# Kernel tuning notes

Hardware: AMD Instinct MI355X
Metric: run time of the kernel (lower is better)

Reference implementation:

```python
import jax, jax.numpy as jnp
import numpy as np
from jax import lax

B, T, IN, H, NCLASS = 256, 512, 64, 128, 6
SCALE = 0.05


def setup_inputs() -> dict:
    key = jax.random.key(0)
    ks = jax.random.split(key, 9)
    return {
        "x": jax.random.normal(ks[0], (B, T, IN), jnp.float32),
        "w_ih0": jax.random.normal(ks[1], (3 * H, IN), jnp.float32) * SCALE,
        "w_ih1": jax.random.normal(ks[2], (3 * H, H), jnp.float32) * SCALE,
        "w_ih2": jax.random.normal(ks[3], (3 * H, H), jnp.float32) * SCALE,
        "w_hh": jax.random.normal(ks[4], (3, 3 * H, H), jnp.float32) * SCALE,
        "b_ih": jax.random.normal(ks[5], (3, 3 * H), jnp.float32) * SCALE,
        "b_hh": jax.random.normal(ks[6], (3, 3 * H), jnp.float32) * SCALE,
        "fc_w": jax.random.normal(ks[7], (NCLASS, H), jnp.float32) * SCALE,
        "fc_b": jax.random.normal(ks[8], (NCLASS,), jnp.float32) * SCALE,
    }


def _gru_layer(x, w_ih, w_hh, b_ih, b_hh):
    # x: [B, T, in]; PyTorch gate order: r, z, n
    gx = jnp.einsum("bti,gi->btg", x, w_ih) + b_ih          # [B, T, 3H]
    gx_r, gx_z, gx_n = jnp.split(gx, 3, axis=-1)
    w_hr, w_hz, w_hn = jnp.split(w_hh, 3, axis=0)           # each [H, H]
    b_hr, b_hz, b_hn = jnp.split(b_hh, 3)

    def step(h, g):
        gr, gz, gn = g
        r = jax.nn.sigmoid(gr + h @ w_hr.T + b_hr)
        z = jax.nn.sigmoid(gz + h @ w_hz.T + b_hz)
        n = jnp.tanh(gn + r * (h @ w_hn.T + b_hn))
        h_new = (1.0 - z) * n + z * h
        return h_new, h_new

    h0 = jnp.zeros((x.shape[0], w_hh.shape[1]), x.dtype)
    xs = (gx_r.transpose(1, 0, 2), gx_z.transpose(1, 0, 2), gx_n.transpose(1, 0, 2))
    _, hs = lax.scan(step, h0, xs)                          # hs: [T, B, H]
    return hs.transpose(1, 0, 2)                            # [B, T, H]


def reference(x, w_ih0, w_ih1, w_ih2, w_hh, b_ih, b_hh, fc_w, fc_b):
    h = _gru_layer(x, w_ih0, w_hh[0], b_ih[0], b_hh[0])
    h = _gru_layer(h, w_ih1, w_hh[1], b_ih[1], b_hh[1])
    h = _gru_layer(h, w_ih2, w_hh[2], b_ih[2], b_hh[2])
    last = h[:, -1, :]                                      # [B, H]
    # Dropout2d(0.25) is identity in eval mode.
    return last @ fc_w.T + fc_b                             # [B, NCLASS]
```

## Files before the change

kernel.cpp:

```cpp
#include <hip/hip_runtime.h>
#include <stdint.h>


#define B_   256
#define T_   512
#define IN_  64
#define H_   128
#define G_   384

typedef short bf16x8 __attribute__((ext_vector_type(8)));
typedef float f32x4  __attribute__((ext_vector_type(4)));
typedef unsigned long long u64x2 __attribute__((ext_vector_type(2)));

__device__ __forceinline__ unsigned short f2bf(float f) {
  union { float f; unsigned u; } v; v.f = f;
  unsigned u = v.u;
  u += 0x7fffu + ((u >> 16) & 1u);
  return (unsigned short)(u >> 16);
}
__device__ __forceinline__ float bf2f(unsigned short h) {
  union { unsigned u; float f; } v; v.u = ((unsigned)h) << 16; return v.f;
}

__device__ __forceinline__ void gload16(const void* g, void* l) {
  __builtin_amdgcn_global_load_lds(
      (const __attribute__((address_space(1))) void*)g,
      (__attribute__((address_space(3))) void*)l, 16, 0, 0);
}

template <int K, bool AF32>
__global__ __launch_bounds__(512) void gemm_gx(const void* __restrict__ Ap,
                                               const float* __restrict__ W,
                                               unsigned short* __restrict__ gx) {
  __shared__ __align__(16) unsigned short smem[(128 + G_) * K];
  unsigned short* lA = smem;
  unsigned short* lW = smem + 128 * K;
  const int tid = threadIdx.x;
  const int m0 = blockIdx.x * 128;

  if (AF32) {
    const float* A = (const float*)Ap;
    const int nch = 128 * K / 4;
    for (int c = tid; c < nch; c += 512) {
      int row = c / (K / 4), kq = c - row * (K / 4);
      float4 v = *(const float4*)(A + (size_t)(m0 + row) * K + kq * 4);
      unsigned long long pk = (unsigned long long)f2bf(v.x) |
                              ((unsigned long long)f2bf(v.y) << 16) |
                              ((unsigned long long)f2bf(v.z) << 32) |
                              ((unsigned long long)f2bf(v.w) << 48);
      unsigned byte = ((unsigned)(row * K + kq * 4) * 2u) ^ (((unsigned)row & 7u) << 4);
      *(unsigned long long*)((char*)lA + byte) = pk;
    }
  } else {
    const unsigned short* A = (const unsigned short*)Ap;
    const int nch = 128 * K / 8;
    for (int c = tid; c < nch; c += 512) {
      int row = c / (K / 8), ko = c - row * (K / 8);
      bf16x8 v = *(const bf16x8*)(A + (size_t)(m0 + row) * K + ko * 8);
      unsigned byte = ((unsigned)(row * K + ko * 8) * 2u) ^ (((unsigned)row & 7u) << 4);
      *(bf16x8*)((char*)lA + byte) = v;
    }
  }
  {
    const int nch = G_ * K / 4;
    for (int c = tid; c < nch; c += 512) {
      int g = c / (K / 4), kq = c - g * (K / 4);
      float4 v = *(const float4*)(W + (size_t)g * K + kq * 4);
      unsigned long long pk = (unsigned long long)f2bf(v.x) |
                              ((unsigned long long)f2bf(v.y) << 16) |
                              ((unsigned long long)f2bf(v.z) << 32) |
                              ((unsigned long long)f2bf(v.w) << 48);
      unsigned byte = ((unsigned)(g * K + kq * 4) * 2u) ^ (((unsigned)g & 7u) << 4);
      *(unsigned long long*)((char*)lW + byte) = pk;
    }
  }
  __syncthreads();

  const int l = tid & 63, w = tid >> 6;
  const int rg = w >> 2, cg = w & 3;
  const int lr = l & 15, g4 = l >> 4;

  f32x4 acc[4][6];
#pragma unroll
  for (int i = 0; i < 4; ++i)
#pragma unroll
    for (int j = 0; j < 6; ++j) acc[i][j] = (f32x4){0.f, 0.f, 0.f, 0.f};

#pragma unroll
  for (int ks = 0; ks < K / 32; ++ks) {
    bf16x8 a[4];
#pragma unroll
    for (int i = 0; i < 4; ++i) {
      int row = (rg * 4 + i) * 16 + lr;
      unsigned byte = ((unsigned)(row * K + ks * 32 + g4 * 8) * 2u) ^ (((unsigned)row & 7u) << 4);
      a[i] = *(const bf16x8*)((const char*)lA + byte);
    }
#pragma unroll
    for (int j = 0; j < 6; ++j) {
      int g = (cg * 6 + j) * 16 + lr;
      unsigned byte = ((unsigned)(g * K + ks * 32 + g4 * 8) * 2u) ^ (((unsigned)g & 7u) << 4);
      bf16x8 bfr = *(const bf16x8*)((const char*)lW + byte);
#pragma unroll
      for (int i = 0; i < 4; ++i)
        acc[i][j] = __builtin_amdgcn_mfma_f32_16x16x32_bf16(a[i], bfr, acc[i][j], 0, 0, 0);
    }
  }

  unsigned short* lC = smem;
#pragma unroll
  for (int half = 0; half < 2; ++half) {
    __syncthreads();
    if (rg == half) {
#pragma unroll
      for (int i = 0; i < 4; ++i)
#pragma unroll
        for (int j = 0; j < 6; ++j)
#pragma unroll
          for (int r = 0; r < 4; ++r) {
            int mloc = i * 16 + g4 * 4 + r;
            int g = (cg * 6 + j) * 16 + lr;
            lC[mloc * 388 + g] = f2bf(acc[i][j][r]);
          }
    }
    __syncthreads();
    for (int it = 0; it < 6; ++it) {
      int c = tid + it * 512;
      int mloc = c / 48, cb = c - mloc * 48;
      unsigned long long lo =
          *(const unsigned long long*)((const char*)lC + mloc * 776 + cb * 16);
      unsigned long long hi =
          *(const unsigned long long*)((const char*)lC + mloc * 776 + cb * 16 + 8);
      int m = m0 + half * 64 + mloc;
      int row;
      if (AF32) { int t = m & 511, b = m >> 9; row = t * 256 + b; }
      else      { row = m; }
      u64x2 v; v[0] = lo; v[1] = hi;
      *(u64x2*)((char*)gx + (size_t)row * (G_ * 2) + cb * 16) = v;
    }
  }
}

template <int DOSEQ, int DOFC>
__global__ __launch_bounds__(512) void gru_scan(
    const unsigned short* __restrict__ gx,
    const float* __restrict__ Whh,
    const float* __restrict__ bih,
    const float* __restrict__ bhh,
    unsigned short* __restrict__ hseq,
    const float* __restrict__ fcw,
    const float* __restrict__ fcb,
    float* __restrict__ out) {
  __shared__ __align__(16) unsigned short lh[2][2048];
  __shared__ __align__(16) unsigned short lgx[4][1536];

  const int tid = threadIdx.x, l = tid & 63, w = tid >> 6;
  const int lr = l & 15, g4 = l >> 4;
  const int b0 = blockIdx.x * 4;
  const int batch = g4;
  const int hcol = w * 16 + lr;

  for (int i = tid; i < 4096; i += 512) ((unsigned short*)lh)[i] = 0;

  const float c_r  = bih[hcol]           + bhh[hcol];
  const float c_z  = bih[128 + hcol]     + bhh[128 + hcol];
  const float c_n1 = bih[256 + hcol];
  const float c_n2 = bhh[256 + hcol];

  bf16x8 Bf[3][4];
#pragma unroll
  for (int ci = 0; ci < 3; ++ci) {
    int gcol = (w + ci * 8) * 16 + lr;
#pragma unroll
    for (int ks = 0; ks < 4; ++ks) {
      const float* p = Whh + (size_t)gcol * H_ + ks * 32 + g4 * 8;
      float4 v0 = *(const float4*)p;
      float4 v1 = *(const float4*)(p + 4);
      bf16x8 f;
      f[0] = (short)f2bf(v0.x); f[1] = (short)f2bf(v0.y);
      f[2] = (short)f2bf(v0.z); f[3] = (short)f2bf(v0.w);
      f[4] = (short)f2bf(v1.x); f[5] = (short)f2bf(v1.y);
      f[6] = (short)f2bf(v1.z); f[7] = (short)f2bf(v1.w);
      Bf[ci][ks] = f;
    }
  }

  __syncthreads();
  if (w < 3) {
#pragma unroll
    for (int p = 0; p < 3; ++p) {
      const char* src = (const char*)gx + ((size_t)(p * 256 + b0) * G_) * 2 + (size_t)tid * 16;
      gload16(src, (char*)&lgx[p][0] + w * 1024);
    }
    asm volatile("s_waitcnt vmcnt(2)" ::: "memory");
  }
  asm volatile("s_waitcnt lgkmcnt(0)" ::: "memory");
  __builtin_amdgcn_s_barrier();
  __builtin_amdgcn_sched_barrier(0);

  float hreg = 0.f;

  for (int t = 0; t < T_; ++t) {
    const int cur = t & 1, nxt = cur ^ 1;
    const int slot = t & 3;

    bf16x8 a[4];
#pragma unroll
    for (int ks = 0; ks < 4; ++ks) {
      unsigned byte = ((unsigned)(lr * 256 + ks * 64 + g4 * 16)) ^ (((unsigned)lr & 7u) << 4);
      a[ks] = *(const bf16x8*)((const char*)lh[cur] + byte);
    }
    const float gxr = bf2f(lgx[slot][batch * G_ + hcol]);
    const float gxz = bf2f(lgx[slot][batch * G_ + 128 + hcol]);
    const float gxn = bf2f(lgx[slot][batch * G_ + 256 + hcol]);

    f32x4 aR = (f32x4){0.f, 0.f, 0.f, 0.f};
    f32x4 aZ = (f32x4){0.f, 0.f, 0.f, 0.f};
    f32x4 aN = (f32x4){0.f, 0.f, 0.f, 0.f};
#pragma unroll
    for (int ks = 0; ks < 4; ++ks) {
      aR = __builtin_amdgcn_mfma_f32_16x16x32_bf16(a[ks], Bf[0][ks], aR, 0, 0, 0);
      aZ = __builtin_amdgcn_mfma_f32_16x16x32_bf16(a[ks], Bf[1][ks], aZ, 0, 0, 0);
      aN = __builtin_amdgcn_mfma_f32_16x16x32_bf16(a[ks], Bf[2][ks], aN, 0, 0, 0);
    }

    float hWr, hWz, hWn;
    {
      float y0 = __shfl(aR[0], lr, 64), y1 = __shfl(aR[1], lr, 64);
      float y2 = __shfl(aR[2], lr, 64), y3 = __shfl(aR[3], lr, 64);
      hWr = batch == 0 ? y0 : batch == 1 ? y1 : batch == 2 ? y2 : y3;
    }
    {
      float y0 = __shfl(aZ[0], lr, 64), y1 = __shfl(aZ[1], lr, 64);
      float y2 = __shfl(aZ[2], lr, 64), y3 = __shfl(aZ[3], lr, 64);
      hWz = batch == 0 ? y0 : batch == 1 ? y1 : batch == 2 ? y2 : y3;
    }
    {
      float y0 = __shfl(aN[0], lr, 64), y1 = __shfl(aN[1], lr, 64);
      float y2 = __shfl(aN[2], lr, 64), y3 = __shfl(aN[3], lr, 64);
      hWn = batch == 0 ? y0 : batch == 1 ? y1 : batch == 2 ? y2 : y3;
    }

    const float rg = 1.f / (1.f + __expf(-(gxr + hWr + c_r)));
    const float zg = 1.f / (1.f + __expf(-(gxz + hWz + c_z)));
    const float nx = gxn + c_n1 + rg * (hWn + c_n2);
    const float ng = 1.f - 2.f / (__expf(2.f * nx) + 1.f);
    hreg = (1.f - zg) * ng + zg * hreg;

    const unsigned short hb = f2bf(hreg);
    *(unsigned short*)((char*)lh[nxt] +
        (((unsigned)(batch * 256 + hcol * 2)) ^ ((unsigned)batch << 4))) = hb;
    if (DOSEQ)
      hseq[(size_t)(t * 256 + b0 + batch) * H_ + hcol] = hb;

    if (w < 3) {
      int t3 = t + 3; if (t3 > T_ - 1) t3 = T_ - 1;
      const char* src = (const char*)gx + ((size_t)(t3 * 256 + b0) * G_) * 2 + (size_t)tid * 16;
      gload16(src, (char*)&lgx[(t + 3) & 3][0] + w * 1024);
    }

    __builtin_amdgcn_sched_barrier(0);
    if (w < 3) {
      asm volatile("s_waitcnt vmcnt(%0)" :: "n"(DOSEQ ? 3 : 2) : "memory");
    }
    asm volatile("s_waitcnt lgkmcnt(0)" ::: "memory");
    __builtin_amdgcn_s_barrier();
    __builtin_amdgcn_sched_barrier(0);
  }

  if (DOFC) {
    __syncthreads();
    float* sc = (float*)&lgx[0][0];
    sc[batch * H_ + hcol] = hreg;
    __syncthreads();
    if (tid < 24) {
      int b = tid / 6, c = tid - b * 6;
      float s = fcb[c];
      for (int k = 0; k < H_; ++k) s += sc[b * H_ + k] * fcw[c * H_ + k];
      out[(size_t)(b0 + b) * 6 + c] = s;
    }
  }
}

extern "C" void kernel_launch(void* const* d_in, const int* in_sizes, int n_in,
                              void* d_out, int out_size, void* d_ws, size_t ws_size,
                              hipStream_t stream) {
  const float* x     = (const float*)d_in[0];
  const float* w_ih0 = (const float*)d_in[1];
  const float* w_ih1 = (const float*)d_in[2];
  const float* w_ih2 = (const float*)d_in[3];
  const float* w_hh  = (const float*)d_in[4];
  const float* b_ih  = (const float*)d_in[5];
  const float* b_hh  = (const float*)d_in[6];
  const float* fc_w  = (const float*)d_in[7];
  const float* fc_b  = (const float*)d_in[8];
  float* out = (float*)d_out;

  unsigned short* gxb  = (unsigned short*)d_ws;
  unsigned short* hseq = gxb + (size_t)T_ * B_ * G_;

  gemm_gx<64, true><<<1024, 512, 0, stream>>>((const void*)x, w_ih0, gxb);
  gru_scan<1, 0><<<64, 512, 0, stream>>>(gxb, w_hh, b_ih, b_hh, hseq,
                                         nullptr, nullptr, nullptr);
  gemm_gx<128, false><<<1024, 512, 0, stream>>>((const void*)hseq, w_ih1, gxb);
  gru_scan<1, 0><<<64, 512, 0, stream>>>(gxb, w_hh + 1 * G_ * H_, b_ih + G_,
                                         b_hh + G_, hseq, nullptr, nullptr, nullptr);
  gemm_gx<128, false><<<1024, 512, 0, stream>>>((const void*)hseq, w_ih2, gxb);
  gru_scan<0, 1><<<64, 512, 0, stream>>>(gxb, w_hh + 2 * G_ * H_, b_ih + 2 * G_,
                                         b_hh + 2 * G_, nullptr, fc_w, fc_b, out);
}
```

Measured before the change: 1.330 ms.

## Fuse GRU layers 0 and 1 into one wavefront-skewed scan kernel

Replaces the layer-0 scan, the layer-1 input-projection GEMM and the layer-1 scan with a single kernel that advances layer 0 at step i and layer 1 at step i-1. The layer-1 input projection is computed per step with MFMA inside the recurrence, so the gx buffer for layer 1 is never written or re-read. Accumulator results are redistributed through an LDS bounce buffer instead of shuffles. The cost is more MFMAs per step on a latency-bound serial loop, roughly triple the register-held weight fragments, and one extra step of skew.

```diff
diff --git a/kernel.cpp b/kernel.cpp
--- a/kernel.cpp
+++ b/kernel.cpp
@@ -26,6 +26,22 @@
   __builtin_amdgcn_global_load_lds(
       (const __attribute__((address_space(1))) void*)g,
       (__attribute__((address_space(3))) void*)l, 16, 0, 0);
+}
+
+__device__ __forceinline__ void load_bfrag(const float* W, int gcol, int g4,
+                                           bf16x8* dst) {
+#pragma unroll
+  for (int ks = 0; ks < 4; ++ks) {
+    const float* p = W + (size_t)gcol * H_ + ks * 32 + g4 * 8;
+    float4 v0 = *(const float4*)p;
+    float4 v1 = *(const float4*)(p + 4);
+    bf16x8 f;
+    f[0] = (short)f2bf(v0.x); f[1] = (short)f2bf(v0.y);
+    f[2] = (short)f2bf(v0.z); f[3] = (short)f2bf(v0.w);
+    f[4] = (short)f2bf(v1.x); f[5] = (short)f2bf(v1.y);
+    f[6] = (short)f2bf(v1.z); f[7] = (short)f2bf(v1.w);
+    dst[ks] = f;
+  }
 }
 
 template <int K, bool AF32>
@@ -140,6 +156,152 @@
   }
 }
 
+__global__ __launch_bounds__(512) void gru_fused01(
+    const unsigned short* __restrict__ gx0,
+    const float* __restrict__ Whh0,
+    const float* __restrict__ Wih1,
+    const float* __restrict__ Whh1,
+    const float* __restrict__ bih,
+    const float* __restrict__ bhh,
+    unsigned short* __restrict__ h1seq) {
+  __shared__ __align__(16) unsigned short lh0[2][512];
+  __shared__ __align__(16) unsigned short lh1[2][512];
+  __shared__ __align__(16) unsigned short lgx[4][1536];
+  __shared__ __align__(16) float bounce[8][7 * 64];
+
+  const int tid = threadIdx.x, l = tid & 63, w = tid >> 6;
+  const int lr = l & 15, g4 = l >> 4;
+  const int b0 = blockIdx.x * 4;
+  const int batch = g4;
+  const int hcol = w * 16 + lr;
+
+  for (int i = tid; i < 2048; i += 512) {
+    ((unsigned short*)lh0)[i & 1023] = 0;
+    ((unsigned short*)lh1)[i & 1023] = 0;
+  }
+
+  const float c0_r  = bih[hcol]       + bhh[hcol];
+  const float c0_z  = bih[128 + hcol] + bhh[128 + hcol];
+  const float c0_n1 = bih[256 + hcol];
+  const float c0_n2 = bhh[256 + hcol];
+  const float c1_r  = bih[G_ + hcol]       + bhh[G_ + hcol];
+  const float c1_z  = bih[G_ + 128 + hcol] + bhh[G_ + 128 + hcol];
+  const float c1_n1 = bih[G_ + 256 + hcol];
+  const float c1_n2 = bhh[G_ + 256 + hcol];
+
+  bf16x8 W0[3][4], Wi[3][4], Wh[3][4];
+#pragma unroll
+  for (int ci = 0; ci < 3; ++ci) {
+    int gcol = (w + ci * 8) * 16 + lr;
+    load_bfrag(Whh0, gcol, g4, W0[ci]);
+    load_bfrag(Wih1, gcol, g4, Wi[ci]);
+    load_bfrag(Whh1, gcol, g4, Wh[ci]);
+  }
+
+  __syncthreads();
+  if (w < 3) {
+#pragma unroll
+    for (int p = 0; p < 3; ++p) {
+      const char* src = (const char*)gx0 + ((size_t)(p * 256 + b0) * G_) * 2 + (size_t)tid * 16;
+      gload16(src, (char*)&lgx[p][0] + w * 1024);
+    }
+    asm volatile("s_waitcnt vmcnt(2)" ::: "memory");
+  }
+  asm volatile("s_waitcnt lgkmcnt(0)" ::: "memory");
+  __builtin_amdgcn_s_barrier();
+  __builtin_amdgcn_sched_barrier(0);
+
+  float h0reg = 0.f, h1reg = 0.f;
+  float* myb = &bounce[w][0];
+
+  for (int i = 0; i <= T_; ++i) {
+    const int cur = i & 1, nxt = cur ^ 1;
+    const int slot = i & 3;
+
+    bf16x8 a0[4], a1[4];
+#pragma unroll
+    for (int ks = 0; ks < 4; ++ks) {
+      unsigned byA = ((unsigned)((lr & 3) * 256 + ks * 64 + g4 * 16)) ^ (((unsigned)lr & 3u) << 4);
+      a0[ks] = *(const bf16x8*)((const char*)lh0[cur] + byA);
+      a1[ks] = *(const bf16x8*)((const char*)lh1[cur] + byA);
+    }
+
+    f32x4 R0 = {0,0,0,0}, Z0 = {0,0,0,0}, N0 = {0,0,0,0};
+    f32x4 R1 = {0,0,0,0}, Z1 = {0,0,0,0}, NX1 = {0,0,0,0}, NH1 = {0,0,0,0};
+#pragma unroll
+    for (int ks = 0; ks < 4; ++ks) {
+      R0 = __builtin_amdgcn_mfma_f32_16x16x32_bf16(a0[ks], W0[0][ks], R0, 0, 0, 0);
+      Z0 = __builtin_amdgcn_mfma_f32_16x16x32_bf16(a0[ks], W0[1][ks], Z0, 0, 0, 0);
+      N0 = __builtin_amdgcn_mfma_f32_16x16x32_bf16(a0[ks], W0[2][ks], N0, 0, 0, 0);
+      R1 = __builtin_amdgcn_mfma_f32_16x16x32_bf16(a0[ks], Wi[0][ks], R1, 0, 0, 0);
+      Z1 = __builtin_amdgcn_mfma_f32_16x16x32_bf16(a0[ks], Wi[1][ks], Z1, 0, 0, 0);
+      NX1 = __builtin_amdgcn_mfma_f32_16x16x32_bf16(a0[ks], Wi[2][ks], NX1, 0, 0, 0);
+      R1 = __builtin_amdgcn_mfma_f32_16x16x32_bf16(a1[ks], Wh[0][ks], R1, 0, 0, 0);
+      Z1 = __builtin_amdgcn_mfma_f32_16x16x32_bf16(a1[ks], Wh[1][ks], Z1, 0, 0, 0);
+      NH1 = __builtin_amdgcn_mfma_f32_16x16x32_bf16(a1[ks], Wh[2][ks], NH1, 0, 0, 0);
+    }
+
+    if (l < 16) {
+      *(f32x4*)(myb + 0 * 64 + lr * 4) = R0;
+      *(f32x4*)(myb + 1 * 64 + lr * 4) = Z0;
+      *(f32x4*)(myb + 2 * 64 + lr * 4) = N0;
+      *(f32x4*)(myb + 3 * 64 + lr * 4) = R1;
+      *(f32x4*)(myb + 4 * 64 + lr * 4) = Z1;
+      *(f32x4*)(myb + 5 * 64 + lr * 4) = NX1;
+      *(f32x4*)(myb + 6 * 64 + lr * 4) = NH1;
+    }
+    asm volatile("s_waitcnt lgkmcnt(0)" ::: "memory");
+    __builtin_amdgcn_sched_barrier(0);
+    const float hWr0 = myb[0 * 64 + lr * 4 + g4];
+    const float hWz0 = myb[1 * 64 + lr * 4 + g4];
+    const float hWn0 = myb[2 * 64 + lr * 4 + g4];
+    const float sR1  = myb[3 * 64 + lr * 4 + g4];
+    const float sZ1  = myb[4 * 64 + lr * 4 + g4];
+    const float sNX1 = myb[5 * 64 + lr * 4 + g4];
+    const float sNH1 = myb[6 * 64 + lr * 4 + g4];
+
+    if (i < T_) {
+      const float gxr = bf2f(lgx[slot][batch * G_ + hcol]);
+      const float gxz = bf2f(lgx[slot][batch * G_ + 128 + hcol]);
+      const float gxn = bf2f(lgx[slot][batch * G_ + 256 + hcol]);
+      const float rg = 1.f / (1.f + __expf(-(gxr + hWr0 + c0_r)));
+      const float zg = 1.f / (1.f + __expf(-(gxz + hWz0 + c0_z)));
+      const float nx = gxn + c0_n1 + rg * (hWn0 + c0_n2);
+      const float ng = 1.f - 2.f / (__expf(2.f * nx) + 1.f);
+      h0reg = (1.f - zg) * ng + zg * h0reg;
+      *(unsigned short*)((char*)lh0[nxt] +
+          (((unsigned)(batch * 256 + hcol * 2)) ^ ((unsigned)batch << 4))) = f2bf(h0reg);
+    }
+
+    if (i > 0) {
+      const float rg = 1.f / (1.f + __expf(-(sR1 + c1_r)));
+      const float zg = 1.f / (1.f + __expf(-(sZ1 + c1_z)));
+      const float nx = sNX1 + c1_n1 + rg * (sNH1 + c1_n2);
+      const float ng = 1.f - 2.f / (__expf(2.f * nx) + 1.f);
+      h1reg = (1.f - zg) * ng + zg * h1reg;
+      const unsigned short hb = f2bf(h1reg);
+      *(unsigned short*)((char*)lh1[nxt] +
+          (((unsigned)(batch * 256 + hcol * 2)) ^ ((unsigned)batch << 4))) = hb;
+      h1seq[(size_t)((i - 1) * 256 + b0 + batch) * H_ + hcol] = hb;
+    }
+
+    if (w < 3) {
+      int t3 = i + 3; if (t3 > T_ - 1) t3 = T_ - 1;
+      const char* src = (const char*)gx0 + ((size_t)(t3 * 256 + b0) * G_) * 2 + (size_t)tid * 16;
+      gload16(src, (char*)&lgx[(i + 3) & 3][0] + w * 1024);
+    }
+
+    __builtin_amdgcn_sched_barrier(0);
+    if (w < 3) {
+      if (i == 0) asm volatile("s_waitcnt vmcnt(2)" ::: "memory");
+      else        asm volatile("s_waitcnt vmcnt(3)" ::: "memory");
+    }
+    asm volatile("s_waitcnt lgkmcnt(0)" ::: "memory");
+    __builtin_amdgcn_s_barrier();
+    __builtin_amdgcn_sched_barrier(0);
+  }
+}
+
 template <int DOSEQ, int DOFC>
 __global__ __launch_bounds__(512) void gru_scan(
     const unsigned short* __restrict__ gx,
@@ -168,21 +330,8 @@
 
   bf16x8 Bf[3][4];
 #pragma unroll
-  for (int ci = 0; ci < 3; ++ci) {
-    int gcol = (w + ci * 8) * 16 + lr;
-#pragma unroll
-    for (int ks = 0; ks < 4; ++ks) {
-      const float* p = Whh + (size_t)gcol * H_ + ks * 32 + g4 * 8;
-      float4 v0 = *(const float4*)p;
-      float4 v1 = *(const float4*)(p + 4);
-      bf16x8 f;
-      f[0] = (short)f2bf(v0.x); f[1] = (short)f2bf(v0.y);
-      f[2] = (short)f2bf(v0.z); f[3] = (short)f2bf(v0.w);
-      f[4] = (short)f2bf(v1.x); f[5] = (short)f2bf(v1.y);
-      f[6] = (short)f2bf(v1.z); f[7] = (short)f2bf(v1.w);
-      Bf[ci][ks] = f;
-    }
-  }
+  for (int ci = 0; ci < 3; ++ci)
+    load_bfrag(Whh, (w + ci * 8) * 16 + lr, g4, Bf[ci]);
 
   __syncthreads();
   if (w < 3) {
@@ -213,9 +362,7 @@
     const float gxz = bf2f(lgx[slot][batch * G_ + 128 + hcol]);
     const float gxn = bf2f(lgx[slot][batch * G_ + 256 + hcol]);
 
-    f32x4 aR = (f32x4){0.f, 0.f, 0.f, 0.f};
-    f32x4 aZ = (f32x4){0.f, 0.f, 0.f, 0.f};
-    f32x4 aN = (f32x4){0.f, 0.f, 0.f, 0.f};
+    f32x4 aR = {0,0,0,0}, aZ = {0,0,0,0}, aN = {0,0,0,0};
 #pragma unroll
     for (int ks = 0; ks < 4; ++ks) {
       aR = __builtin_amdgcn_mfma_f32_16x16x32_bf16(a[ks], Bf[0][ks], aR, 0, 0, 0);
@@ -299,11 +446,8 @@
   unsigned short* hseq = gxb + (size_t)T_ * B_ * G_;
 
   gemm_gx<64, true><<<1024, 512, 0, stream>>>((const void*)x, w_ih0, gxb);
-  gru_scan<1, 0><<<64, 512, 0, stream>>>(gxb, w_hh, b_ih, b_hh, hseq,
-                                         nullptr, nullptr, nullptr);
-  gemm_gx<128, false><<<1024, 512, 0, stream>>>((const void*)hseq, w_ih1, gxb);
-  gru_scan<1, 0><<<64, 512, 0, stream>>>(gxb, w_hh + 1 * G_ * H_, b_ih + G_,
-                                         b_hh + G_, hseq, nullptr, nullptr, nullptr);
+  gru_fused01<<<64, 512, 0, stream>>>(gxb, w_hh, w_ih1, w_hh + 1 * G_ * H_,
+                                      b_ih, b_hh, hseq);
   gemm_gx<128, false><<<1024, 512, 0, stream>>>((const void*)hseq, w_ih2, gxb);
   gru_scan<0, 1><<<64, 512, 0, stream>>>(gxb, w_hh + 2 * G_ * H_, b_ih + 2 * G_,
                                          b_hh + 2 * G_, nullptr, fc_w, fc_b, out);
```

Measured after the change: 1.452 ms. 1.09x slower.
